# Performance work log

Hardware: AMD Instinct MI355X
Metric: run time of the kernel (lower is better)

The kernel has to match this reference:

```python
import jax, jax.numpy as jnp
from jax import lax
import numpy as np

DATA_CHANNELS = 3
CIN = 256
S = 256  # out_channels / split_size / LSTM hidden
B, H, W = 32, 64, 64
DN = ('NCHW', 'OIHW', 'NCHW')


def build_mask_B(out_c, in_c, dc):
    # MaskedConv2d mask for kernel (1,3), type 'B': yc=0, xc=1.
    m = np.zeros((out_c, in_c, 1, 3), dtype=np.float32)
    m[:, :, 0, :2] = 1.0  # columns 0,1 allowed; column 2 (future) zeroed
    oc = np.arange(out_c) % dc
    ic = np.arange(in_c) % dc
    bad = oc[:, None] < ic[None, :]  # in-data-channel ahead of out-data-channel
    center = m[:, :, 0, 1]
    center[bad] = 0.0
    m[:, :, 0, 1] = center
    return jnp.asarray(m)


def setup_inputs() -> dict:
    key = jax.random.key(0)
    ks = jax.random.split(key, 8)
    sc = 0.05
    return {
        'x': jax.random.normal(ks[0], (B, CIN, H, W), dtype=jnp.float32),
        'w_i2s': jax.random.normal(ks[1], (S, CIN, 1, 3), dtype=jnp.float32) * sc,
        'b_i2s': jax.random.normal(ks[2], (S,), dtype=jnp.float32) * sc,
        'w_s2s': jax.random.normal(ks[3], (S, S, 1, 3), dtype=jnp.float32) * sc,
        'b_s2s': jax.random.normal(ks[4], (S,), dtype=jnp.float32) * sc,
        'w_ih': jax.random.normal(ks[5], (4 * S, S), dtype=jnp.float32) * sc,
        'b_ih': jax.random.normal(ks[6], (4 * S,), dtype=jnp.float32) * sc,
        'b_hh': jax.random.normal(ks[7], (4 * S,), dtype=jnp.float32) * sc,
    }


def reference(x, w_i2s, b_i2s, w_s2s, b_s2s, w_ih, b_ih, b_hh):
    b, cin, h_dim, w_dim = x.shape
    s = w_i2s.shape[0]
    mask = build_mask_B(s, cin, DATA_CHANNELS)
    # input-to-state masked conv (1,3), pad (0,1): (B, S, H, W)
    xs = lax.conv_general_dilated(x, w_i2s * mask, (1, 1), [(0, 0), (1, 1)],
                                  dimension_numbers=DN) + b_i2s[None, :, None, None]
    # per-row flattened inputs, matching torch permute(0,2,1).view(-1,1,S): (H, B*W, S)
    x_rows = jnp.transpose(xs, (2, 0, 3, 1)).reshape(h_dim, b * w_dim, s)
    bias = b_ih + b_hh  # h_prev is zeroed each step, so W_hh term vanishes; biases remain

    def step(carry, x_row):
        h, c = carry  # each (B*W, S)
        # state-to-state conv over the flattened B*W axis (faithful to original layout)
        hc = lax.conv_general_dilated(h.T[None, :, None, :], w_s2s, (1, 1),
                                      [(0, 0), (1, 1)], dimension_numbers=DN)
        hc = hc[0, :, 0, :].T + b_s2s  # (B*W, S)
        gates = (x_row + hc) @ w_ih.T + bias  # (B*W, 4S)
        i, f, g, o = jnp.split(gates, 4, axis=-1)
        c = jax.nn.sigmoid(f) * c + jax.nn.sigmoid(i) * jnp.tanh(g)
        h = jax.nn.sigmoid(o) * jnp.tanh(c)
        return (h, c), h

    init = (jnp.zeros((b * w_dim, s), x.dtype), jnp.zeros((b * w_dim, s), x.dtype))
    _, hs = lax.scan(step, init, x_rows)  # (H, B*W, S)
    # torch does h.view(B, S, 1, W): a raw row-major reshape of the (B*W, S) buffer
    out = hs.reshape(h_dim, b, s, w_dim)
    return jnp.transpose(out, (1, 2, 0, 3))  # (B, S, H, W)
```

## Files before the change

### kernel.cpp

```cpp
#include <hip/hip_runtime.h>
#include <math.h>

#define BATCH 32
#define CINCH 256
#define SDIM  256
#define HDIM  64
#define WDIM  64
#define BW    (BATCH*WDIM)
#define NGATE (4*SDIM)

#define XS_OFF   0ull
#define H_OFF    (XS_OFF  + (size_t)HDIM*BW*SDIM)
#define C_OFF    (H_OFF   + (size_t)BW*SDIM)
#define T_OFF    (C_OFF   + (size_t)BW*SDIM)
#define WR_OFF   (T_OFF   + (size_t)BW*SDIM)
#define CB_OFF   (WR_OFF  + (size_t)NGATE*SDIM)
#define WT0_OFF  (CB_OFF  + (size_t)NGATE)
#define WT1_OFF  (WT0_OFF + (size_t)CINCH*SDIM)
#define WST_OFF  (WT1_OFF + (size_t)CINCH*SDIM)
#define WS_TOTAL (WST_OFF + (size_t)SDIM*3*SDIM)

typedef __attribute__((ext_vector_type(8))) short bf16x8;
typedef __attribute__((ext_vector_type(4))) float f32x4;

__device__ __forceinline__ ushort f2bf(float f) {
  uint u = __float_as_uint(f);
  u += 0x7fffu + ((u >> 16) & 1u);
  return (ushort)(u >> 16);
}
__device__ __forceinline__ float bf2f(ushort b) {
  return __uint_as_float(((uint)b) << 16);
}
__device__ __forceinline__ float sigf(float v) { return 1.f / (1.f + expf(-v)); }

__global__ void prep_kernel(const float* __restrict__ w_i2s,
                            const float* __restrict__ w_s2s,
                            const float* __restrict__ w_ih,
                            const float* __restrict__ b_ih,
                            const float* __restrict__ b_hh,
                            float* __restrict__ ws) {
  float* wt0 = ws + WT0_OFF;
  float* wt1 = ws + WT1_OFF;
  float* wst = ws + WST_OFF;
  ushort* whi = (ushort*)(ws + WR_OFF);
  ushort* wlo = whi + (size_t)NGATE * SDIM;
  float* cbn = ws + CB_OFF;
  int idx = blockIdx.x * blockDim.x + threadIdx.x;
  int stride = gridDim.x * blockDim.x;

  for (int i = idx; i < CINCH * SDIM; i += stride) {
    int ic = i >> 8;
    int s  = i & 255;
    wt0[i] = w_i2s[(s * CINCH + ic) * 3 + 0];
    float cw = w_i2s[(s * CINCH + ic) * 3 + 1];
    wt1[i] = ((s % 3) >= (ic % 3)) ? cw : 0.f;
  }
  for (int i = idx; i < SDIM * 3 * SDIM; i += stride) {
    int s  = i & 255;
    int ut = i >> 8;
    int t  = ut % 3;
    int u  = ut / 3;
    wst[i] = w_s2s[(s * SDIM + u) * 3 + t];
  }
  for (int i = idx; i < NGATE * SDIM; i += stride) {
    int r   = i & 7;
    int ln  = (i >> 3) & 63;
    int ks  = (i >> 9) & 7;
    int gt  = i >> 12;
    int g   = gt >> 4;
    int t16 = gt & 15;
    int sp  = t16 * 16 + (ln & 15);
    int k   = ks * 32 + (ln >> 4) * 8 + r;
    float v = w_ih[((size_t)(g * SDIM + sp)) * SDIM + k];
    ushort hi = f2bf(v);
    whi[i] = hi;
    wlo[i] = f2bf(v - bf2f(hi));
  }
  for (int i = idx; i < NGATE; i += stride) cbn[i] = b_ih[i] + b_hh[i];
}

__global__ __launch_bounds__(512) void i2s_kernel(const float* __restrict__ x,
                                                  const float* __restrict__ b_i2s,
                                                  const float* __restrict__ wt0,
                                                  const float* __restrict__ wt1,
                                                  float* __restrict__ xs) {
  __shared__ float xl[CINCH * WDIM];
  const int b = blockIdx.x & 31;
  const int h = blockIdx.x >> 5;
  const int tid = threadIdx.x;

  const float* xb = x + ((size_t)b * CINCH * HDIM + h) * WDIM;
  for (int i4 = tid; i4 < CINCH * WDIM / 4; i4 += 512) {
    int ic = i4 >> 4;
    int w4 = i4 & 15;
    float4 v = *(const float4*)(xb + (size_t)ic * HDIM * WDIM + w4 * 4);
    *(float4*)(&xl[ic * WDIM + w4 * 4]) = v;
  }
  __syncthreads();

  const int s    = tid & 255;
  const int half = tid >> 8;
  float acc[32];
#pragma unroll
  for (int w = 0; w < 32; ++w) acc[w] = 0.f;

  for (int ic = 0; ic < CINCH; ++ic) {
    float w0 = wt0[ic * SDIM + s];
    float w1 = wt1[ic * SDIM + s];
    const float4* xr4 = (const float4*)(&xl[ic * WDIM + half * 32]);
    float prev = half ? xl[ic * WDIM + 31] : 0.f;
#pragma unroll
    for (int q = 0; q < 8; ++q) {
      float4 v = xr4[q];
      acc[4 * q + 0] += w0 * prev + w1 * v.x;
      acc[4 * q + 1] += w0 * v.x  + w1 * v.y;
      acc[4 * q + 2] += w0 * v.y  + w1 * v.z;
      acc[4 * q + 3] += w0 * v.z  + w1 * v.w;
      prev = v.w;
    }
  }
  float bias = b_i2s[s];
  float* xsrow = xs + ((size_t)(h * BW + b * WDIM) + half * 32) * SDIM + s;
#pragma unroll
  for (int w = 0; w < 32; ++w) xsrow[(size_t)w * SDIM] = acc[w] + bias;
}

__global__ __launch_bounds__(256) void hc2_kernel(const float* __restrict__ h,
                                                  const float* __restrict__ wst,
                                                  const float* __restrict__ xs_step,
                                                  const float* __restrict__ b_s2s,
                                                  ushort* __restrict__ thi,
                                                  ushort* __restrict__ tlo) {
  __shared__ float hl[32 * 34];
  __shared__ float Bsh[32 * 192];
  const int p0 = blockIdx.x * 32;
  const int s0 = blockIdx.y * 64;
  const int tid = threadIdx.x;
  const int tx = tid & 15;
  const int ty = tid >> 4;

  float acc[2][4];
#pragma unroll
  for (int r = 0; r < 2; ++r)
#pragma unroll
    for (int cc = 0; cc < 4; ++cc) acc[r][cc] = 0.f;

  for (int kt = 0; kt < 8; ++kt) {
    const int u0 = kt * 32;
    __syncthreads();
    for (int i = tid; i < 32 * 34; i += 256) {
      int u_l = i & 31;
      int j   = i >> 5;
      int p   = p0 - 1 + j;
      hl[u_l * 34 + j] = (p < 0 || p >= BW) ? 0.f : h[(size_t)p * SDIM + u0 + u_l];
    }
    for (int i = tid; i < 1536; i += 256) {
      int u_l = i / 48;
      int rem = i - u_l * 48;
      int t   = rem >> 4;
      int s4  = rem & 15;
      float4 v = *(const float4*)(wst + (size_t)(u0 + u_l) * 768 + t * 256 + s0 + s4 * 4);
      *(float4*)(&Bsh[u_l * 192 + t * 64 + s4 * 4]) = v;
    }
    __syncthreads();
#pragma unroll 8
    for (int u = 0; u < 32; ++u) {
      const float* hb = &hl[u * 34 + ty * 2];
      float a[4] = {hb[0], hb[1], hb[2], hb[3]};
      float4 b0 = *(const float4*)(&Bsh[u * 192 + tx * 4]);
      float4 b1 = *(const float4*)(&Bsh[u * 192 + 64 + tx * 4]);
      float4 b2 = *(const float4*)(&Bsh[u * 192 + 128 + tx * 4]);
      float B0[4] = {b0.x, b0.y, b0.z, b0.w};
      float B1[4] = {b1.x, b1.y, b1.z, b1.w};
      float B2[4] = {b2.x, b2.y, b2.z, b2.w};
#pragma unroll
      for (int r = 0; r < 2; ++r)
#pragma unroll
        for (int cc = 0; cc < 4; ++cc)
          acc[r][cc] += B0[cc] * a[r] + B1[cc] * a[r + 1] + B2[cc] * a[r + 2];
    }
  }

  float4 bs4 = *(const float4*)(b_s2s + s0 + tx * 4);
#pragma unroll
  for (int r = 0; r < 2; ++r) {
    int p = p0 + ty * 2 + r;
    float4 xv = *(const float4*)(xs_step + (size_t)p * SDIM + s0 + tx * 4);
    float v0 = acc[r][0] + bs4.x + xv.x;
    float v1 = acc[r][1] + bs4.y + xv.y;
    float v2 = acc[r][2] + bs4.z + xv.z;
    float v3 = acc[r][3] + bs4.w + xv.w;
    ushort h0 = f2bf(v0), h1 = f2bf(v1), h2 = f2bf(v2), h3 = f2bf(v3);
    uint2 ph; ph.x = (uint)h0 | ((uint)h1 << 16); ph.y = (uint)h2 | ((uint)h3 << 16);
    ushort l0 = f2bf(v0 - bf2f(h0)), l1 = f2bf(v1 - bf2f(h1));
    ushort l2 = f2bf(v2 - bf2f(h2)), l3 = f2bf(v3 - bf2f(h3));
    uint2 pl; pl.x = (uint)l0 | ((uint)l1 << 16); pl.y = (uint)l2 | ((uint)l3 << 16);
    size_t off = (size_t)p * SDIM + s0 + tx * 4;
    *(uint2*)(thi + off) = ph;
    *(uint2*)(tlo + off) = pl;
  }
}

__global__ __launch_bounds__(256) void gates_mfma_kernel(
    const ushort* __restrict__ t_hi, const ushort* __restrict__ t_lo,
    const ushort* __restrict__ w_hi, const ushort* __restrict__ w_lo,
    const float* __restrict__ cbn,
    float* __restrict__ h, float* __restrict__ c,
    float* __restrict__ out, int step) {
  __shared__ ushort Ah[32 * 264];
  __shared__ ushort Al[32 * 264];
  const int p0 = blockIdx.x * 32;
  const int s0 = blockIdx.y * 64;
  const int tid  = threadIdx.x;
  const int lane = tid & 63;
  const int wid  = tid >> 6;

  for (int it = 0; it < 4; ++it) {
    int idx8 = it * 256 + tid;
    int row  = idx8 >> 5;
    int k8   = (idx8 & 31) * 8;
    size_t goff = (size_t)(p0 + row) * SDIM + k8;
    uint4 vh = *(const uint4*)(t_hi + goff);
    uint4 vl = *(const uint4*)(t_lo + goff);
    *(uint4*)(&Ah[row * 264 + k8]) = vh;
    *(uint4*)(&Al[row * 264 + k8]) = vl;
  }
  __syncthreads();

  const int l15 = lane & 15;
  const int kg  = lane >> 4;
  const int t16 = (s0 >> 4) + wid;

  f32x4 zero = {0.f, 0.f, 0.f, 0.f};
  f32x4 acc[2][4];
#pragma unroll
  for (int sb = 0; sb < 2; ++sb)
#pragma unroll
    for (int g = 0; g < 4; ++g) acc[sb][g] = zero;

#pragma unroll
  for (int ks = 0; ks < 8; ++ks) {
    bf16x8 ah[2], al[2];
#pragma unroll
    for (int sb = 0; sb < 2; ++sb) {
      int ao = (sb * 16 + l15) * 264 + ks * 32 + kg * 8;
      ah[sb] = *(const bf16x8*)(&Ah[ao]);
      al[sb] = *(const bf16x8*)(&Al[ao]);
    }
#pragma unroll
    for (int g = 0; g < 4; ++g) {
      size_t bo = ((((size_t)(g * 16 + t16)) * 8 + ks) * 64 + lane) * 8;
      bf16x8 bh = *(const bf16x8*)(w_hi + bo);
      bf16x8 bl = *(const bf16x8*)(w_lo + bo);
#pragma unroll
      for (int sb = 0; sb < 2; ++sb) {
        acc[sb][g] = __builtin_amdgcn_mfma_f32_16x16x32_bf16(ah[sb], bh, acc[sb][g], 0, 0, 0);
        acc[sb][g] = __builtin_amdgcn_mfma_f32_16x16x32_bf16(ah[sb], bl, acc[sb][g], 0, 0, 0);
        acc[sb][g] = __builtin_amdgcn_mfma_f32_16x16x32_bf16(al[sb], bh, acc[sb][g], 0, 0, 0);
      }
    }
  }

  const int sp = s0 + wid * 16 + l15;
  float cbi = cbn[sp], cbf = cbn[256 + sp], cbg = cbn[512 + sp], cbo = cbn[768 + sp];
#pragma unroll
  for (int sb = 0; sb < 2; ++sb) {
#pragma unroll
    for (int r = 0; r < 4; ++r) {
      int p = p0 + sb * 16 + kg * 4 + r;
      float gi = acc[sb][0][r] + cbi;
      float gf = acc[sb][1][r] + cbf;
      float gg = acc[sb][2][r] + cbg;
      float go = acc[sb][3][r] + cbo;
      float cold = c[(size_t)p * SDIM + sp];
      float cn = sigf(gf) * cold + sigf(gi) * tanhf(gg);
      float hn = sigf(go) * tanhf(cn);
      c[(size_t)p * SDIM + sp] = cn;
      h[(size_t)p * SDIM + sp] = hn;
      int bb = p >> 6;
      int w  = p & 63;
      int s2 = (w << 2) | (sp >> 6);
      int w2 = sp & 63;
      out[(((size_t)bb * SDIM + s2) * HDIM + step) * WDIM + w2] = hn;
    }
  }
}

extern "C" void kernel_launch(void* const* d_in, const int* in_sizes, int n_in,
                              void* d_out, int out_size, void* d_ws, size_t ws_size,
                              hipStream_t stream) {
  const float* x     = (const float*)d_in[0];
  const float* w_i2s = (const float*)d_in[1];
  const float* b_i2s = (const float*)d_in[2];
  const float* w_s2s = (const float*)d_in[3];
  const float* b_s2s = (const float*)d_in[4];
  const float* w_ih  = (const float*)d_in[5];
  const float* b_ih  = (const float*)d_in[6];
  const float* b_hh  = (const float*)d_in[7];
  float* out = (float*)d_out;
  float* ws  = (float*)d_ws;
  (void)in_sizes; (void)n_in; (void)out_size; (void)ws_size;

  ushort* thi = (ushort*)(ws + T_OFF);
  ushort* tlo = thi + (size_t)BW * SDIM;
  ushort* whi = (ushort*)(ws + WR_OFF);
  ushort* wlo = whi + (size_t)NGATE * SDIM;

  prep_kernel<<<512, 256, 0, stream>>>(w_i2s, w_s2s, w_ih, b_ih, b_hh, ws);
  i2s_kernel<<<HDIM * BATCH, 512, 0, stream>>>(x, b_i2s, ws + WT0_OFF, ws + WT1_OFF,
                                               ws + XS_OFF);
  hipMemsetAsync(ws + H_OFF, 0, 2 * (size_t)BW * SDIM * sizeof(float), stream);

  for (int step = 0; step < HDIM; ++step) {
    hc2_kernel<<<dim3(BW / 32, SDIM / 64), 256, 0, stream>>>(
        ws + H_OFF, ws + WST_OFF, ws + XS_OFF + (size_t)step * BW * SDIM, b_s2s,
        thi, tlo);
    gates_mfma_kernel<<<dim3(BW / 32, SDIM / 64), 256, 0, stream>>>(
        thi, tlo, whi, wlo, ws + CB_OFF, ws + H_OFF, ws + C_OFF, out, step);
  }
}
```

Before: 4.486 ms.

## Fold state-to-state conv into gate GEMM via precomputed W_ih·W_s2s weights

Precomputes the product of W_ih with the reshaped s2s conv weights, plus a folded bias, in extra prep kernels. Each recurrence step then becomes one fused MFMA kernel that multiplies the concatenated [xs, h shifted -1, h, h shifted +1] against the combined weights. This removes the per-step fp32 hc2 kernel and its intermediate round-trip through global memory. The cost is a four-times-larger K dimension in the split-bf16 MFMA GEMM, and h and xs are now stored as bf16 hi/lo pairs with ping-pong h buffers.

```diff
diff --git a/kernel.cpp b/kernel.cpp
--- a/kernel.cpp
+++ b/kernel.cpp
@@ -6,19 +6,23 @@
 #define SDIM  256
 #define HDIM  64
 #define WDIM  64
-#define BW    (BATCH*WDIM)
-#define NGATE (4*SDIM)
-
-#define XS_OFF   0ull
-#define H_OFF    (XS_OFF  + (size_t)HDIM*BW*SDIM)
-#define C_OFF    (H_OFF   + (size_t)BW*SDIM)
-#define T_OFF    (C_OFF   + (size_t)BW*SDIM)
-#define WR_OFF   (T_OFF   + (size_t)BW*SDIM)
-#define CB_OFF   (WR_OFF  + (size_t)NGATE*SDIM)
-#define WT0_OFF  (CB_OFF  + (size_t)NGATE)
-#define WT1_OFF  (WT0_OFF + (size_t)CINCH*SDIM)
-#define WST_OFF  (WT1_OFF + (size_t)CINCH*SDIM)
-#define WS_TOTAL (WST_OFF + (size_t)SDIM*3*SDIM)
+#define BW    2048
+#define NGATE 1024
+
+#define XSH_OFF  0ull
+#define XSL_OFF  (XSH_OFF + 16777216ull)
+#define HH0_OFF  (XSL_OFF + 16777216ull)
+#define HL0_OFF  (HH0_OFF + 262144ull)
+#define HH1_OFF  (HL0_OFF + 262144ull)
+#define HL1_OFF  (HH1_OFF + 262144ull)
+#define C_OFF    (HL1_OFF + 262144ull)
+#define WFH_OFF  (C_OFF + 524288ull)
+#define WFL_OFF  (WFH_OFF + 524288ull)
+#define CB_OFF   (WFL_OFF + 524288ull)
+#define WT0_OFF  (CB_OFF + 1024ull)
+#define WT1_OFF  (WT0_OFF + 65536ull)
+#define W2B_OFF  XSH_OFF
+#define WS2R_OFF (XSH_OFF + 786432ull)
 
 typedef __attribute__((ext_vector_type(8))) short bf16x8;
 typedef __attribute__((ext_vector_type(4))) float f32x4;
@@ -33,18 +37,19 @@
 }
 __device__ __forceinline__ float sigf(float v) { return 1.f / (1.f + expf(-v)); }
 
-__global__ void prep_kernel(const float* __restrict__ w_i2s,
-                            const float* __restrict__ w_s2s,
-                            const float* __restrict__ w_ih,
-                            const float* __restrict__ b_ih,
-                            const float* __restrict__ b_hh,
-                            float* __restrict__ ws) {
+__global__ void prep0_kernel(const float* __restrict__ w_i2s,
+                             const float* __restrict__ w_s2s,
+                             const float* __restrict__ w_ih,
+                             const float* __restrict__ b_ih,
+                             const float* __restrict__ b_hh,
+                             const float* __restrict__ b_s2s,
+                             float* __restrict__ ws) {
   float* wt0 = ws + WT0_OFF;
   float* wt1 = ws + WT1_OFF;
-  float* wst = ws + WST_OFF;
-  ushort* whi = (ushort*)(ws + WR_OFF);
-  ushort* wlo = whi + (size_t)NGATE * SDIM;
-  float* cbn = ws + CB_OFF;
+  float* ws2r = ws + WS2R_OFF;
+  float* cb  = ws + CB_OFF;
+  ushort* whi = (ushort*)(ws + WFH_OFF);
+  ushort* wlo = (ushort*)(ws + WFL_OFF);
   int idx = blockIdx.x * blockDim.x + threadIdx.x;
   int stride = gridDim.x * blockDim.x;
 
@@ -55,35 +60,113 @@
     float cw = w_i2s[(s * CINCH + ic) * 3 + 1];
     wt1[i] = ((s % 3) >= (ic % 3)) ? cw : 0.f;
   }
-  for (int i = idx; i < SDIM * 3 * SDIM; i += stride) {
-    int s  = i & 255;
-    int ut = i >> 8;
-    int t  = ut % 3;
-    int u  = ut / 3;
-    wst[i] = w_s2s[(s * SDIM + u) * 3 + t];
+  for (int i = idx; i < SDIM * 768; i += stride) {
+    int s = i / 768;
+    int rem = i - s * 768;
+    int t = rem >> 8;
+    int u = rem & 255;
+    ws2r[i] = w_s2s[((size_t)s * SDIM + u) * 3 + t];
   }
   for (int i = idx; i < NGATE * SDIM; i += stride) {
     int r   = i & 7;
     int ln  = (i >> 3) & 63;
     int ks  = (i >> 9) & 7;
-    int gt  = i >> 12;
-    int g   = gt >> 4;
-    int t16 = gt & 15;
-    int sp  = t16 * 16 + (ln & 15);
-    int k   = ks * 32 + (ln >> 4) * 8 + r;
-    float v = w_ih[((size_t)(g * SDIM + sp)) * SDIM + k];
+    int j16 = i >> 12;
+    int j = (j16 >> 4) * 256 + (j16 & 15) * 16 + (ln & 15);
+    int k = ks * 32 + (ln >> 4) * 8 + r;
+    float v = w_ih[(size_t)j * SDIM + k];
     ushort hi = f2bf(v);
-    whi[i] = hi;
-    wlo[i] = f2bf(v - bf2f(hi));
-  }
-  for (int i = idx; i < NGATE; i += stride) cbn[i] = b_ih[i] + b_hh[i];
+    size_t flat = (((size_t)j16 * 32 + ks) * 64 + ln) * 8 + r;
+    whi[flat] = hi;
+    wlo[flat] = f2bf(v - bf2f(hi));
+  }
+  for (int j = idx; j < NGATE; j += stride) {
+    float a = b_ih[j] + b_hh[j];
+    const float* wr = w_ih + (size_t)j * SDIM;
+    for (int s = 0; s < SDIM; ++s) a += wr[s] * b_s2s[s];
+    cb[j] = a;
+  }
+}
+
+__global__ __launch_bounds__(256) void prep1_kernel(const float* __restrict__ w_ih,
+                                                    const float* __restrict__ ws2r,
+                                                    float* __restrict__ w2b) {
+  __shared__ float As[16 * 64];
+  __shared__ float Bs[16 * 64];
+  const int j0 = blockIdx.x * 64;
+  const int n0 = blockIdx.y * 64;
+  const int tid = threadIdx.x;
+  const int tx = tid & 15;
+  const int ty = tid >> 4;
+
+  float acc[4][4];
+#pragma unroll
+  for (int r = 0; r < 4; ++r)
+#pragma unroll
+    for (int cc = 0; cc < 4; ++cc) acc[r][cc] = 0.f;
+
+  const int lrow = tid >> 2;
+  const int lk4  = tid & 3;
+  const int bkl  = tid >> 4;
+  const int bn4  = tid & 15;
+
+  for (int kt = 0; kt < 16; ++kt) {
+    const int k0 = kt * 16;
+    float4 av = *(const float4*)(w_ih + (size_t)(j0 + lrow) * SDIM + k0 + lk4 * 4);
+    float4 bv = *(const float4*)(ws2r + (size_t)(k0 + bkl) * 768 + n0 + bn4 * 4);
+    __syncthreads();
+    As[(lk4 * 4 + 0) * 64 + lrow] = av.x;
+    As[(lk4 * 4 + 1) * 64 + lrow] = av.y;
+    As[(lk4 * 4 + 2) * 64 + lrow] = av.z;
+    As[(lk4 * 4 + 3) * 64 + lrow] = av.w;
+    *(float4*)(&Bs[bkl * 64 + bn4 * 4]) = bv;
+    __syncthreads();
+#pragma unroll
+    for (int kk = 0; kk < 16; ++kk) {
+      float4 a = *(const float4*)(&As[kk * 64 + ty * 4]);
+      float4 b = *(const float4*)(&Bs[kk * 64 + tx * 4]);
+      float ar[4] = {a.x, a.y, a.z, a.w};
+      float br[4] = {b.x, b.y, b.z, b.w};
+#pragma unroll
+      for (int r = 0; r < 4; ++r)
+#pragma unroll
+        for (int cc = 0; cc < 4; ++cc) acc[r][cc] += ar[r] * br[cc];
+    }
+  }
+#pragma unroll
+  for (int r = 0; r < 4; ++r)
+#pragma unroll
+    for (int cc = 0; cc < 4; ++cc)
+      w2b[(size_t)(j0 + ty * 4 + r) * 768 + n0 + tx * 4 + cc] = acc[r][cc];
+}
+
+__global__ void prep2_kernel(const float* __restrict__ w2b, float* __restrict__ ws) {
+  ushort* whi = (ushort*)(ws + WFH_OFF);
+  ushort* wlo = (ushort*)(ws + WFL_OFF);
+  int idx = blockIdx.x * blockDim.x + threadIdx.x;
+  int stride = gridDim.x * blockDim.x;
+  for (int i = idx; i < NGATE * 768; i += stride) {
+    int r  = i & 7;
+    int ln = (i >> 3) & 63;
+    int t1 = i >> 9;
+    int ksg8 = t1 % 24;
+    int j16  = t1 / 24;
+    int j  = (j16 >> 4) * 256 + (j16 & 15) * 16 + (ln & 15);
+    int k2 = ksg8 * 32 + (ln >> 4) * 8 + r;
+    float v = w2b[(size_t)j * 768 + k2];
+    ushort hi = f2bf(v);
+    size_t flat = (((size_t)j16 * 32 + 8 + ksg8) * 64 + ln) * 8 + r;
+    whi[flat] = hi;
+    wlo[flat] = f2bf(v - bf2f(hi));
+  }
 }
 
 __global__ __launch_bounds__(512) void i2s_kernel(const float* __restrict__ x,
                                                   const float* __restrict__ b_i2s,
                                                   const float* __restrict__ wt0,
                                                   const float* __restrict__ wt1,
-                                                  float* __restrict__ xs) {
+                                                  ushort* __restrict__ xs_hi,
+                                                  ushort* __restrict__ xs_lo) {
   __shared__ float xl[CINCH * WDIM];
   const int b = blockIdx.x & 31;
   const int h = blockIdx.x >> 5;
@@ -120,92 +203,22 @@
     }
   }
   float bias = b_i2s[s];
-  float* xsrow = xs + ((size_t)(h * BW + b * WDIM) + half * 32) * SDIM + s;
-#pragma unroll
-  for (int w = 0; w < 32; ++w) xsrow[(size_t)w * SDIM] = acc[w] + bias;
-}
-
-__global__ __launch_bounds__(256) void hc2_kernel(const float* __restrict__ h,
-                                                  const float* __restrict__ wst,
-                                                  const float* __restrict__ xs_step,
-                                                  const float* __restrict__ b_s2s,
-                                                  ushort* __restrict__ thi,
-                                                  ushort* __restrict__ tlo) {
-  __shared__ float hl[32 * 34];
-  __shared__ float Bsh[32 * 192];
-  const int p0 = blockIdx.x * 32;
-  const int s0 = blockIdx.y * 64;
-  const int tid = threadIdx.x;
-  const int tx = tid & 15;
-  const int ty = tid >> 4;
-
-  float acc[2][4];
-#pragma unroll
-  for (int r = 0; r < 2; ++r)
-#pragma unroll
-    for (int cc = 0; cc < 4; ++cc) acc[r][cc] = 0.f;
-
-  for (int kt = 0; kt < 8; ++kt) {
-    const int u0 = kt * 32;
-    __syncthreads();
-    for (int i = tid; i < 32 * 34; i += 256) {
-      int u_l = i & 31;
-      int j   = i >> 5;
-      int p   = p0 - 1 + j;
-      hl[u_l * 34 + j] = (p < 0 || p >= BW) ? 0.f : h[(size_t)p * SDIM + u0 + u_l];
-    }
-    for (int i = tid; i < 1536; i += 256) {
-      int u_l = i / 48;
-      int rem = i - u_l * 48;
-      int t   = rem >> 4;
-      int s4  = rem & 15;
-      float4 v = *(const float4*)(wst + (size_t)(u0 + u_l) * 768 + t * 256 + s0 + s4 * 4);
-      *(float4*)(&Bsh[u_l * 192 + t * 64 + s4 * 4]) = v;
-    }
-    __syncthreads();
-#pragma unroll 8
-    for (int u = 0; u < 32; ++u) {
-      const float* hb = &hl[u * 34 + ty * 2];
-      float a[4] = {hb[0], hb[1], hb[2], hb[3]};
-      float4 b0 = *(const float4*)(&Bsh[u * 192 + tx * 4]);
-      float4 b1 = *(const float4*)(&Bsh[u * 192 + 64 + tx * 4]);
-      float4 b2 = *(const float4*)(&Bsh[u * 192 + 128 + tx * 4]);
-      float B0[4] = {b0.x, b0.y, b0.z, b0.w};
-      float B1[4] = {b1.x, b1.y, b1.z, b1.w};
-      float B2[4] = {b2.x, b2.y, b2.z, b2.w};
-#pragma unroll
-      for (int r = 0; r < 2; ++r)
-#pragma unroll
-        for (int cc = 0; cc < 4; ++cc)
-          acc[r][cc] += B0[cc] * a[r] + B1[cc] * a[r + 1] + B2[cc] * a[r + 2];
-    }
-  }
-
-  float4 bs4 = *(const float4*)(b_s2s + s0 + tx * 4);
-#pragma unroll
-  for (int r = 0; r < 2; ++r) {
-    int p = p0 + ty * 2 + r;
-    float4 xv = *(const float4*)(xs_step + (size_t)p * SDIM + s0 + tx * 4);
-    float v0 = acc[r][0] + bs4.x + xv.x;
-    float v1 = acc[r][1] + bs4.y + xv.y;
-    float v2 = acc[r][2] + bs4.z + xv.z;
-    float v3 = acc[r][3] + bs4.w + xv.w;
-    ushort h0 = f2bf(v0), h1 = f2bf(v1), h2 = f2bf(v2), h3 = f2bf(v3);
-    uint2 ph; ph.x = (uint)h0 | ((uint)h1 << 16); ph.y = (uint)h2 | ((uint)h3 << 16);
-    ushort l0 = f2bf(v0 - bf2f(h0)), l1 = f2bf(v1 - bf2f(h1));
-    ushort l2 = f2bf(v2 - bf2f(h2)), l3 = f2bf(v3 - bf2f(h3));
-    uint2 pl; pl.x = (uint)l0 | ((uint)l1 << 16); pl.y = (uint)l2 | ((uint)l3 << 16);
-    size_t off = (size_t)p * SDIM + s0 + tx * 4;
-    *(uint2*)(thi + off) = ph;
-    *(uint2*)(tlo + off) = pl;
-  }
-}
-
-__global__ __launch_bounds__(256) void gates_mfma_kernel(
-    const ushort* __restrict__ t_hi, const ushort* __restrict__ t_lo,
+  size_t base = ((size_t)(h * BW + b * WDIM) + half * 32) * SDIM + s;
+#pragma unroll
+  for (int w = 0; w < 32; ++w) {
+    float v = acc[w] + bias;
+    ushort hi = f2bf(v);
+    xs_hi[base + (size_t)w * SDIM] = hi;
+    xs_lo[base + (size_t)w * SDIM] = f2bf(v - bf2f(hi));
+  }
+}
+
+__global__ __launch_bounds__(256) void gates_fused_kernel(
+    const ushort* __restrict__ xs_hi_step, const ushort* __restrict__ xs_lo_step,
+    const ushort* __restrict__ h_hi_rd, const ushort* __restrict__ h_lo_rd,
+    ushort* __restrict__ h_hi_wr, ushort* __restrict__ h_lo_wr,
     const ushort* __restrict__ w_hi, const ushort* __restrict__ w_lo,
-    const float* __restrict__ cbn,
-    float* __restrict__ h, float* __restrict__ c,
+    const float* __restrict__ cbn, float* __restrict__ c,
     float* __restrict__ out, int step) {
   __shared__ ushort Ah[32 * 264];
   __shared__ ushort Al[32 * 264];
@@ -214,19 +227,6 @@
   const int tid  = threadIdx.x;
   const int lane = tid & 63;
   const int wid  = tid >> 6;
-
-  for (int it = 0; it < 4; ++it) {
-    int idx8 = it * 256 + tid;
-    int row  = idx8 >> 5;
-    int k8   = (idx8 & 31) * 8;
-    size_t goff = (size_t)(p0 + row) * SDIM + k8;
-    uint4 vh = *(const uint4*)(t_hi + goff);
-    uint4 vl = *(const uint4*)(t_lo + goff);
-    *(uint4*)(&Ah[row * 264 + k8]) = vh;
-    *(uint4*)(&Al[row * 264 + k8]) = vl;
-  }
-  __syncthreads();
-
   const int l15 = lane & 15;
   const int kg  = lane >> 4;
   const int t16 = (s0 >> 4) + wid;
@@ -238,25 +238,54 @@
 #pragma unroll
     for (int g = 0; g < 4; ++g) acc[sb][g] = zero;
 
-#pragma unroll
-  for (int ks = 0; ks < 8; ++ks) {
-    bf16x8 ah[2], al[2];
-#pragma unroll
-    for (int sb = 0; sb < 2; ++sb) {
-      int ao = (sb * 16 + l15) * 264 + ks * 32 + kg * 8;
-      ah[sb] = *(const bf16x8*)(&Ah[ao]);
-      al[sb] = *(const bf16x8*)(&Al[ao]);
-    }
-#pragma unroll
-    for (int g = 0; g < 4; ++g) {
-      size_t bo = ((((size_t)(g * 16 + t16)) * 8 + ks) * 64 + lane) * 8;
-      bf16x8 bh = *(const bf16x8*)(w_hi + bo);
-      bf16x8 bl = *(const bf16x8*)(w_lo + bo);
+  for (int tc = 0; tc < 4; ++tc) {
+    __syncthreads();
+#pragma unroll
+    for (int it = 0; it < 4; ++it) {
+      int idx8 = it * 256 + tid;
+      int row  = idx8 >> 5;
+      int k8   = (idx8 & 31) * 8;
+      uint4 vh, vl;
+      if (tc == 0) {
+        size_t off = (size_t)(p0 + row) * SDIM + k8;
+        vh = *(const uint4*)(xs_hi_step + off);
+        vl = *(const uint4*)(xs_lo_step + off);
+      } else {
+        int pr = p0 + row + tc - 2;
+        if (pr >= 0 && pr < BW) {
+          size_t off = (size_t)pr * SDIM + k8;
+          vh = *(const uint4*)(h_hi_rd + off);
+          vl = *(const uint4*)(h_lo_rd + off);
+        } else {
+          vh = make_uint4(0, 0, 0, 0);
+          vl = make_uint4(0, 0, 0, 0);
+        }
+      }
+      *(uint4*)(&Ah[row * 264 + k8]) = vh;
+      *(uint4*)(&Al[row * 264 + k8]) = vl;
+    }
+    __syncthreads();
+#pragma unroll
+    for (int ks = 0; ks < 8; ++ks) {
+      bf16x8 ah[2], al[2];
 #pragma unroll
       for (int sb = 0; sb < 2; ++sb) {
-        acc[sb][g] = __builtin_amdgcn_mfma_f32_16x16x32_bf16(ah[sb], bh, acc[sb][g], 0, 0, 0);
-        acc[sb][g] = __builtin_amdgcn_mfma_f32_16x16x32_bf16(ah[sb], bl, acc[sb][g], 0, 0, 0);
-        acc[sb][g] = __builtin_amdgcn_mfma_f32_16x16x32_bf16(al[sb], bh, acc[sb][g], 0, 0, 0);
+        int ao = (sb * 16 + l15) * 264 + ks * 32 + kg * 8;
+        ah[sb] = *(const bf16x8*)(&Ah[ao]);
+        al[sb] = *(const bf16x8*)(&Al[ao]);
+      }
+      const int ksg = tc * 8 + ks;
+#pragma unroll
+      for (int g = 0; g < 4; ++g) {
+        size_t bo = ((((size_t)(g * 16 + t16)) * 32 + ksg) * 64 + lane) * 8;
+        bf16x8 bh = *(const bf16x8*)(w_hi + bo);
+        bf16x8 bl = *(const bf16x8*)(w_lo + bo);
+#pragma unroll
+        for (int sb = 0; sb < 2; ++sb) {
+          acc[sb][g] = __builtin_amdgcn_mfma_f32_16x16x32_bf16(ah[sb], bh, acc[sb][g], 0, 0, 0);
+          acc[sb][g] = __builtin_amdgcn_mfma_f32_16x16x32_bf16(ah[sb], bl, acc[sb][g], 0, 0, 0);
+          acc[sb][g] = __builtin_amdgcn_mfma_f32_16x16x32_bf16(al[sb], bh, acc[sb][g], 0, 0, 0);
+        }
       }
     }
   }
@@ -276,7 +305,9 @@
       float cn = sigf(gf) * cold + sigf(gi) * tanhf(gg);
       float hn = sigf(go) * tanhf(cn);
       c[(size_t)p * SDIM + sp] = cn;
-      h[(size_t)p * SDIM + sp] = hn;
+      ushort hh = f2bf(hn);
+      h_hi_wr[(size_t)p * SDIM + sp] = hh;
+      h_lo_wr[(size_t)p * SDIM + sp] = f2bf(hn - bf2f(hh));
       int bb = p >> 6;
       int w  = p & 63;
       int s2 = (w << 2) | (sp >> 6);
@@ -301,21 +332,29 @@
   float* ws  = (float*)d_ws;
   (void)in_sizes; (void)n_in; (void)out_size; (void)ws_size;
 
-  ushort* thi = (ushort*)(ws + T_OFF);
-  ushort* tlo = thi + (size_t)BW * SDIM;
-  ushort* whi = (ushort*)(ws + WR_OFF);
-  ushort* wlo = whi + (size_t)NGATE * SDIM;
-
-  prep_kernel<<<512, 256, 0, stream>>>(w_i2s, w_s2s, w_ih, b_ih, b_hh, ws);
+  ushort* xs_hi = (ushort*)(ws + XSH_OFF);
+  ushort* xs_lo = (ushort*)(ws + XSL_OFF);
+  ushort* h_hi0 = (ushort*)(ws + HH0_OFF);
+  ushort* h_lo0 = (ushort*)(ws + HL0_OFF);
+  ushort* h_hi1 = (ushort*)(ws + HH1_OFF);
+  ushort* h_lo1 = (ushort*)(ws + HL1_OFF);
+  ushort* w_hi  = (ushort*)(ws + WFH_OFF);
+  ushort* w_lo  = (ushort*)(ws + WFL_OFF);
+  float*  w2b   = ws + W2B_OFF;
+
+  prep0_kernel<<<256, 256, 0, stream>>>(w_i2s, w_s2s, w_ih, b_ih, b_hh, b_s2s, ws);
+  prep1_kernel<<<dim3(16, 12), 256, 0, stream>>>(w_ih, ws + WS2R_OFF, w2b);
+  prep2_kernel<<<384, 256, 0, stream>>>(w2b, ws);
   i2s_kernel<<<HDIM * BATCH, 512, 0, stream>>>(x, b_i2s, ws + WT0_OFF, ws + WT1_OFF,
-                                               ws + XS_OFF);
-  hipMemsetAsync(ws + H_OFF, 0, 2 * (size_t)BW * SDIM * sizeof(float), stream);
+                                               xs_hi, xs_lo);
+  hipMemsetAsync(ws + HH0_OFF, 0, (4ull * 262144 + 524288) * 4, stream);
 
   for (int step = 0; step < HDIM; ++step) {
-    hc2_kernel<<<dim3(BW / 32, SDIM / 64), 256, 0, stream>>>(
-        ws + H_OFF, ws + WST_OFF, ws + XS_OFF + (size_t)step * BW * SDIM, b_s2s,
-        thi, tlo);
-    gates_mfma_kernel<<<dim3(BW / 32, SDIM / 64), 256, 0, stream>>>(
-        thi, tlo, whi, wlo, ws + CB_OFF, ws + H_OFF, ws + C_OFF, out, step);
-  }
-}
+    const int par = step & 1;
+    gates_fused_kernel<<<dim3(BW / 32, SDIM / 64), 256, 0, stream>>>(
+        xs_hi + (size_t)step * BW * SDIM, xs_lo + (size_t)step * BW * SDIM,
+        par ? h_hi1 : h_hi0, par ? h_lo1 : h_lo0,
+        par ? h_hi0 : h_hi1, par ? h_lo0 : h_lo1,
+        w_hi, w_lo, ws + CB_OFF, ws + C_OFF, out, step);
+  }
+}
```

Result: faster. 3.876 ms (-13.6%).
